# Kernel tuning notes

Measured on AMD Instinct MI355X. Metric: run time of the kernel, lower is better.

## Reference

```python
import jax, jax.numpy as jnp
import numpy as np

T = 20            # time_steps
BETA = 0.85
THR = 1.0         # snntorch Leaky default threshold
A_PRE = 0.005
A_POST = -0.003
STDP_INT = 3


@jax.custom_vjp
def spike_fn(mem_shift):
    # heaviside spike; backward uses snntorch atan surrogate (alpha=2)
    return (mem_shift > 0).astype(mem_shift.dtype)

def _spk_fwd(m):
    return (m > 0).astype(m.dtype), m

def _spk_bwd(m, g):
    # snntorch surrogate.atan, alpha=2: grad = g * (alpha/2) / (1 + (pi/2*alpha*U)^2) = g / (1 + (pi*U)^2)
    return (g / (1.0 + (jnp.pi * m) ** 2),)

spike_fn.defvjp(_spk_fwd, _spk_bwd)


def _lif(cur, mem):
    # snntorch Leaky (reset-by-subtraction): reset from previous mem (detached)
    reset = jax.lax.stop_gradient((mem > THR).astype(cur.dtype))
    mem = BETA * mem + cur - reset * THR
    spk = spike_fn(mem - THR)
    return spk, mem


def _snn_forward(x, embed, W1, b1, W2, b2, W3, b3, Wout, bout):
    B, S = x.shape
    H = W1.shape[0]
    x_emb = jnp.transpose(embed[x], (1, 0, 2))   # [S,B,E]
    x_rep = jnp.repeat(x_emb, T, axis=0)         # [S*T,B,E] (same embed for all 20 steps of a token)

    def step(carry, xe):
        mem1, mem2, mem3 = carry
        spk1, mem1 = _lif(xe @ W1.T + b1, mem1)
        spk2, mem2 = _lif(spk1 @ W2.T + b2, mem2)
        spk3, mem3 = _lif(spk2 @ W3.T + b3, mem3)
        return (mem1, mem2, mem3), (spk1, spk2, spk3)

    z = jnp.zeros((B, H), x_emb.dtype)
    (mem1, mem2, mem3), (spk1a, spk2a, spk3a) = jax.lax.scan(step, (z, z, z), x_rep)

    # STDP accumulation on steps where step % 3 == 0 (no-grad in original)
    mask = jnp.tile((jnp.arange(T) % STDP_INT == 0).astype(x_emb.dtype), S)  # [S*T]

    def stdp(pre, post):
        pre_m = jax.lax.stop_gradient(pre.mean(axis=1))    # [N, in]
        post_m = jax.lax.stop_gradient(post.mean(axis=1))  # [N, out]
        return jnp.einsum('n,no,ni->oi', mask, A_POST * post_m, A_PRE * pre_m)

    d1 = stdp(x_rep, spk1a)
    d2 = stdp(spk1a, spk2a)
    d3 = stdp(spk2a, spk3a)

    pooled = spk3a.reshape(S, T, B, H).mean(axis=1)  # mean over time_steps -> [S,B,H]
    out = jnp.transpose(pooled @ Wout.T + bout, (1, 0, 2))  # [B,S,V]
    rec1, rec2, rec3 = (jax.lax.stop_gradient(s) for s in (spk1a, spk2a, spk3a))
    return out, mem1, mem2, mem3, d1, d2, d3, rec1, rec2, rec3


def setup_inputs() -> dict:
    key = jax.random.key(0)
    ks = jax.random.split(key, 10)
    V, H, E, B, S = 32000, 256, 128, 32, 128
    inp = {
        'x': jax.random.randint(ks[0], (B, S), 0, V),
        'embed': jax.random.normal(ks[1], (V, E), jnp.float32),
        'W1': jax.random.normal(ks[2], (H, E), jnp.float32) * 0.08,
        'b1': jnp.zeros((H,), jnp.float32),
        'W2': jax.random.normal(ks[3], (H, H), jnp.float32) * 0.06,
        'b2': jnp.zeros((H,), jnp.float32),
        'W3': jax.random.normal(ks[4], (H, H), jnp.float32) * 0.06,
        'b3': jnp.zeros((H,), jnp.float32),
        'Wout': jax.random.normal(ks[5], (V, H), jnp.float32) * 0.06,
        'bout': jnp.zeros((V,), jnp.float32),
    }
    return inp


def reference(x, embed, W1, b1, W2, b2, W3, b3, Wout, bout):
    return _snn_forward(x, embed, W1, b1, W2, b2, W3, b3, Wout, bout)
```

## Files before the change

### kernel.cpp

```cpp
#include <hip/hip_runtime.h>
#include <cstdint>

#define T_STEPS 20
#define S_LEN   128
#define BATCH   32
#define HID     256
#define EMB     128
#define VOCAB   32000
#define NSTEP   (S_LEN*T_STEPS)
#define NBROWS  (NSTEP*BATCH)

typedef __bf16 bf8   __attribute__((ext_vector_type(8)));
typedef float  f32x4 __attribute__((ext_vector_type(4)));

static __device__ __forceinline__ unsigned short f2bf_u(float f){
  unsigned int u = __builtin_bit_cast(unsigned int, f);
  u = u + 0x7FFFu + ((u >> 16) & 1u);
  return (unsigned short)(u >> 16);
}

__global__ void k_f32_to_bf16(const float* __restrict__ src, unsigned short* __restrict__ dst, int n4){
  int i = blockIdx.x*blockDim.x + threadIdx.x;
  if (i < n4){
    float4 v = ((const float4*)src)[i];
    ushort4 o; o.x=f2bf_u(v.x); o.y=f2bf_u(v.y); o.z=f2bf_u(v.z); o.w=f2bf_u(v.w);
    ((ushort4*)dst)[i] = o;
  }
}

__global__ void k_wT(const float* __restrict__ W, float* __restrict__ WT){
  int i = blockIdx.x*blockDim.x + threadIdx.x;
  int n = i >> 8, k = i & 255;
  WT[k*HID + n] = W[i];
}

__global__ void k_xm(const int* __restrict__ x, const float* __restrict__ embed, float* __restrict__ Xm){
  int s = blockIdx.x, i = threadIdx.x;
  float acc = 0.f;
  for (int b=0;b<BATCH;b++){
    int tok = x[b*S_LEN + s];
    acc += embed[(size_t)tok*EMB + i];
  }
  Xm[s*EMB + i] = acc * (1.0f/32.0f);
}

__global__ __launch_bounds__(256) void k_cur1(const int* __restrict__ x, const float* __restrict__ embed,
                                              const float* __restrict__ W1, const float* __restrict__ b1,
                                              float* __restrict__ cur1){
  __shared__ float xe[BATCH*EMB];
  int s = blockIdx.x, t = threadIdx.x;
  for (int i=t; i<BATCH*EMB/4; i+=256){
    int b = i >> 5, e4 = i & 31;
    int tok = x[b*S_LEN + s];
    ((float4*)xe)[i] = ((const float4*)(embed + (size_t)tok*EMB))[e4];
  }
  __syncthreads();
  int h = t;
  float acc[BATCH];
  #pragma unroll
  for (int b=0;b<BATCH;b++) acc[b]=0.f;
  for (int ec=0; ec<4; ec++){
    float wd[32];
    #pragma unroll
    for (int e4=0;e4<8;e4++){
      float4 w = *(const float4*)(W1 + (size_t)h*EMB + ec*32 + e4*4);
      wd[e4*4+0]=w.x; wd[e4*4+1]=w.y; wd[e4*4+2]=w.z; wd[e4*4+3]=w.w;
    }
    #pragma unroll
    for (int b=0;b<BATCH;b++){
      #pragma unroll
      for (int e=0;e<32;e++)
        acc[b] = fmaf(xe[b*EMB + ec*32 + e], wd[e], acc[b]);
    }
  }
  float bi = b1[h];
  #pragma unroll
  for (int b=0;b<BATCH;b++)
    cur1[(size_t)(s*BATCH + b)*HID + h] = __fadd_rn(acc[b], bi);
}

__global__ __launch_bounds__(64) void k_scan1(const float* __restrict__ cur1, float* __restrict__ rec,
                                              float* __restrict__ memout){
  int bid = blockIdx.x; int b = bid >> 2; int hq = bid & 3;
  int h = hq*64 + threadIdx.x;
  const int strN = BATCH*HID;
  const float* cp = cur1 + b*HID + h;
  float* rp = rec + b*HID + h;
  float mem = 0.f;
  float c = cp[0];
  for (int s=0; s<S_LEN; s++){
    float cn = (s+1 < S_LEN) ? cp[(size_t)(s+1)*strN] : 0.f;
    #pragma unroll
    for (int t=0;t<T_STEPS;t++){
      float reset = (mem > 1.0f) ? 1.0f : 0.0f;
      float tm = __fmul_rn(0.85f, mem);
      tm = __fadd_rn(tm, c);
      mem = __fsub_rn(tm, reset);
      rp[(size_t)(s*T_STEPS + t)*strN] = (mem > 1.0f) ? 1.0f : 0.0f;
    }
    c = cn;
  }
  memout[b*HID + h] = mem;
}

template<bool POOL>
__global__ __launch_bounds__(64) void k_scan23(const float* __restrict__ cur,
                                               float* __restrict__ rec, float* __restrict__ memout,
                                               unsigned short* __restrict__ pooled){
  int bid = blockIdx.x; int b = bid >> 2; int hq = bid & 3;
  int h = hq*64 + threadIdx.x;
  const int strN = BATCH*HID;
  const float* cp = cur + b*HID + h;
  float* rp = rec + b*HID + h;
  unsigned short* pp = POOL ? (pooled + (size_t)b*S_LEN*HID + h) : nullptr;
  float mem = 0.f;
  float ps = 0.f;
  int tc = 0, sTok = 0;
  float cA[16], cB[16];

  auto step = [&](float c, int n){
    float reset = (mem > 1.0f) ? 1.0f : 0.0f;
    float tm = __fmul_rn(0.85f, mem);
    tm = __fadd_rn(tm, c);
    mem = __fsub_rn(tm, reset);
    float spk = (mem > 1.0f) ? 1.f : 0.f;
    rp[(size_t)n*strN] = spk;
    if constexpr (POOL){
      ps += spk;
      if (++tc == T_STEPS){
        pp[(size_t)sTok*HID] = f2bf_u(__fdiv_rn(ps, 20.0f));
        ps = 0.f; tc = 0; ++sTok;
      }
    }
  };

  #pragma unroll
  for (int j=0;j<16;j++) cA[j] = cp[(size_t)j*strN];
  for (int n0=0; n0<NSTEP; n0+=32){
    #pragma unroll
    for (int j=0;j<16;j++) cB[j] = cp[(size_t)(n0+16+j)*strN];
    #pragma unroll
    for (int j=0;j<16;j++) step(cA[j], n0+j);
    if (n0+32 < NSTEP){
      #pragma unroll
      for (int j=0;j<16;j++) cA[j] = cp[(size_t)(n0+32+j)*strN];
    }
    #pragma unroll
    for (int j=0;j<16;j++) step(cB[j], n0+16+j);
  }
  memout[b*HID + h] = mem;
}

__global__ __launch_bounds__(256) void k_gemm_f32(const float* __restrict__ spk,
                                                  const float* __restrict__ WT,
                                                  const float* __restrict__ bias,
                                                  float* __restrict__ curo){
  __shared__ float As[256*36];
  int m0 = blockIdx.y * 256;
  int n0 = blockIdx.x * 32;
  int t  = threadIdx.x;
  float acc[32];
  #pragma unroll
  for (int n=0;n<32;n++) acc[n]=0.f;

  for (int kc=0; kc<8; kc++){
    __syncthreads();
    #pragma unroll
    for (int i=0;i<8;i++){
      int id = t + i*256;
      int r = id >> 3, c4 = id & 7;
      float4 v = *(const float4*)(spk + (size_t)(m0 + r)*HID + kc*32 + c4*4);
      *(float4*)(As + r*36 + c4*4) = v;
    }
    __syncthreads();
    const float* wrow = WT + (size_t)(kc*32)*HID + n0;
    #pragma unroll
    for (int g=0; g<8; g++){
      float4 sv4 = *(const float4*)(As + t*36 + g*4);
      #pragma unroll
      for (int j=0;j<4;j++){
        float sv = (j==0)?sv4.x:(j==1)?sv4.y:(j==2)?sv4.z:sv4.w;
        const float* wt = wrow + (size_t)(g*4+j)*HID;
        #pragma unroll
        for (int n=0;n<32;n++)
          acc[n] = fmaf(sv, wt[n], acc[n]);
      }
    }
  }
  float* op = curo + (size_t)(m0 + t)*HID + n0;
  #pragma unroll
  for (int n=0;n<32;n++) op[n] = __fadd_rn(acc[n], bias[n0+n]);
}

template<bool BF16B>
__global__ __launch_bounds__(256,2) void k_gemm_out(const unsigned short* __restrict__ Abf,
                                                    const unsigned short* __restrict__ Bbf,
                                                    const float* __restrict__ Bf32,
                                                    const float* __restrict__ bout,
                                                    float* __restrict__ outp){
  __shared__ unsigned short As[128*72];
  __shared__ unsigned short Bs[128*72];
  int bid = blockIdx.x;
  int ntile = bid >> 5;
  int mtile = bid & 31;
  int m0 = mtile*128, n0 = ntile*128;
  int tid = threadIdx.x;
  int lane = tid & 63, wave = tid >> 6;
  int wm = wave >> 1, wn = wave & 1;
  int lm = lane & 15, quad = lane >> 4;
  f32x4 acc[4][4] = {};

  for (int kt=0; kt<4; kt++){
    int k0 = kt*64;
    uint4 avb[4];
    #pragma unroll
    for (int i=0;i<4;i++){
      int id = tid + i*256; int r = id>>3, c16 = id&7;
      avb[i] = *(const uint4*)(Abf + (size_t)(m0 + r)*HID + k0 + c16*8);
    }
    uint4 bvb[4]; float4 bvf[8];
    if (BF16B){
      #pragma unroll
      for (int i=0;i<4;i++){
        int id = tid + i*256; int r = id>>3, c16 = id&7;
        bvb[i] = *(const uint4*)(Bbf + (size_t)(n0 + r)*HID + k0 + c16*8);
      }
    } else {
      #pragma unroll
      for (int i=0;i<8;i++){
        int id = tid + i*256; int r = id>>4, c4 = id&15;
        bvf[i] = *(const float4*)(Bf32 + (size_t)(n0 + r)*HID + k0 + c4*4);
      }
    }
    __syncthreads();
    #pragma unroll
    for (int i=0;i<4;i++){
      int id = tid + i*256; int r = id>>3, c16 = id&7;
      *(uint4*)(As + r*72 + c16*8) = avb[i];
    }
    if (BF16B){
      #pragma unroll
      for (int i=0;i<4;i++){
        int id = tid + i*256; int r = id>>3, c16 = id&7;
        *(uint4*)(Bs + r*72 + c16*8) = bvb[i];
      }
    } else {
      #pragma unroll
      for (int i=0;i<8;i++){
        int id = tid + i*256; int r = id>>4, c4 = id&15;
        ushort4 o; o.x=f2bf_u(bvf[i].x); o.y=f2bf_u(bvf[i].y); o.z=f2bf_u(bvf[i].z); o.w=f2bf_u(bvf[i].w);
        *(ushort4*)(Bs + r*72 + c4*4) = o;
      }
    }
    __syncthreads();
    bf8 af[4][2], bfr[4][2];
    #pragma unroll
    for (int mt=0;mt<4;mt++)
      #pragma unroll
      for (int kk=0;kk<2;kk++)
        af[mt][kk] = *(const bf8*)(As + (wm*64 + mt*16 + lm)*72 + kk*32 + quad*8);
    #pragma unroll
    for (int nt=0;nt<4;nt++)
      #pragma unroll
      for (int kk=0;kk<2;kk++)
        bfr[nt][kk] = *(const bf8*)(Bs + (wn*64 + nt*16 + lm)*72 + kk*32 + quad*8);
    #pragma unroll
    for (int mt=0;mt<4;mt++)
      #pragma unroll
      for (int nt=0;nt<4;nt++){
        acc[mt][nt] = __builtin_amdgcn_mfma_f32_16x16x32_bf16(af[mt][0], bfr[nt][0], acc[mt][nt], 0,0,0);
        acc[mt][nt] = __builtin_amdgcn_mfma_f32_16x16x32_bf16(af[mt][1], bfr[nt][1], acc[mt][nt], 0,0,0);
      }
    __syncthreads();
  }
  #pragma unroll
  for (int nt=0;nt<4;nt++){
    int v = n0 + wn*64 + nt*16 + lm;
    float bo = bout[v];
    #pragma unroll
    for (int mt=0;mt<4;mt++)
      #pragma unroll
      for (int rr=0;rr<4;rr++){
        int r = m0 + wm*64 + mt*16 + quad*4 + rr;
        outp[(size_t)r*VOCAB + v] = acc[mt][nt][rr] + bo;
      }
  }
}

__global__ void k_mmean(const float* __restrict__ rec, float* __restrict__ M){
  int m = blockIdx.x, o = threadIdx.x;
  int s = m / 7, j = m - 7*s;
  int n = s*T_STEPS + j*3;
  const float* rp = rec + (size_t)n*BATCH*HID + o;
  float acc = 0.f;
  #pragma unroll
  for (int b=0;b<BATCH;b++) acc += rp[b*HID];
  M[m*HID + o] = acc * (1.0f/32.0f);
}

__global__ void k_d1(const float* __restrict__ M1, const float* __restrict__ Xm, float* __restrict__ d1){
  __shared__ float col[896];
  int o = blockIdx.x, i = threadIdx.x;
  for (int m=i; m<896; m+=128) col[m] = M1[m*HID + o];
  __syncthreads();
  float acc = 0.f;
  for (int s=0;s<S_LEN;s++){
    float xv = Xm[s*EMB + i];
    float cs = 0.f;
    #pragma unroll
    for (int j=0;j<7;j++) cs += col[s*7+j];
    acc += cs * xv;
  }
  d1[o*EMB + i] = -1.5e-5f * acc;
}

__global__ void k_d23(const float* __restrict__ Mpost, const float* __restrict__ Mpre, float* __restrict__ d){
  __shared__ float col[896];
  int o = blockIdx.x, i = threadIdx.x;
  for (int m=i; m<896; m+=256) col[m] = Mpost[m*HID + o];
  __syncthreads();
  float acc = 0.f;
  for (int m=0;m<896;m++) acc += col[m] * Mpre[m*HID + i];
  d[o*HID + i] = -1.5e-5f * acc;
}

extern "C" void kernel_launch(void* const* d_in, const int* in_sizes, int n_in,
                              void* d_out, int out_size, void* d_ws, size_t ws_size,
                              hipStream_t stream){
  const int*   x     = (const int*)d_in[0];
  const float* embed = (const float*)d_in[1];
  const float* W1    = (const float*)d_in[2];
  const float* b1    = (const float*)d_in[3];
  const float* W2    = (const float*)d_in[4];
  const float* b2    = (const float*)d_in[5];
  const float* W3    = (const float*)d_in[6];
  const float* b3    = (const float*)d_in[7];
  const float* Wout  = (const float*)d_in[8];
  const float* bout  = (const float*)d_in[9];
  float* out = (float*)d_out;

  float* mem1 = out + 131072000;
  float* mem2 = out + 131080192;
  float* mem3 = out + 131088384;
  float* d1   = out + 131096576;
  float* d2   = out + 131129344;
  float* d3   = out + 131194880;
  float* rec1 = out + 131260416;
  float* rec2 = out + 152231936;
  float* rec3 = out + 173203456;

  float* curbuf = out + 0;
  float* cur1   = out + 20971520;
  float* Xm     = out + 22020096;
  float* M1     = out + 22036480;
  float* M2     = out + 22265856;
  float* M3     = out + 22495232;
  float* WT2    = out + 22724608;
  float* WT3    = out + 22790144;

  unsigned short* pooled = (unsigned short*)d_ws;
  bool haveWoutBf = ws_size >= (size_t)(2097152 + 16384000);
  unsigned short* woutbf = (unsigned short*)((char*)d_ws + 2097152);

  if (haveWoutBf)
    k_f32_to_bf16<<<8000,256,0,stream>>>(Wout, woutbf, VOCAB*HID/4);
  k_wT<<<256,256,0,stream>>>(W2, WT2);
  k_wT<<<256,256,0,stream>>>(W3, WT3);
  k_xm<<<128,128,0,stream>>>(x, embed, Xm);
  k_cur1<<<128,256,0,stream>>>(x, embed, W1, b1, cur1);

  k_scan1<<<128,64,0,stream>>>(cur1, rec1, mem1);
  k_gemm_f32<<<dim3(8,320),256,0,stream>>>(rec1, WT2, b2, curbuf);
  k_scan23<false><<<128,64,0,stream>>>(curbuf, rec2, mem2, nullptr);
  k_gemm_f32<<<dim3(8,320),256,0,stream>>>(rec2, WT3, b3, curbuf);
  k_scan23<true><<<128,64,0,stream>>>(curbuf, rec3, mem3, pooled);

  k_mmean<<<896,256,0,stream>>>(rec1, M1);
  k_mmean<<<896,256,0,stream>>>(rec2, M2);
  k_mmean<<<896,256,0,stream>>>(rec3, M3);
  k_d1<<<256,128,0,stream>>>(M1, Xm, d1);
  k_d23<<<256,256,0,stream>>>(M2, M1, d2);
  k_d23<<<256,256,0,stream>>>(M3, M2, d3);

  if (haveWoutBf)
    k_gemm_out<true ><<<8000,256,0,stream>>>(pooled, woutbf, nullptr, bout, out);
  else
    k_gemm_out<false><<<8000,256,0,stream>>>(pooled, nullptr, Wout,  bout, out);
}
```

Measured before the change: 1.966 ms.

## Fuse prep kernels, remap GEMM blocks per XCD, use nontemporal output stores

```diff
diff --git a/kernel.cpp b/kernel.cpp
--- a/kernel.cpp
+++ b/kernel.cpp
@@ -19,29 +19,36 @@
   return (unsigned short)(u >> 16);
 }
 
-__global__ void k_f32_to_bf16(const float* __restrict__ src, unsigned short* __restrict__ dst, int n4){
-  int i = blockIdx.x*blockDim.x + threadIdx.x;
-  if (i < n4){
-    float4 v = ((const float4*)src)[i];
+__global__ __launch_bounds__(256) void k_prep(const float* __restrict__ Wout, unsigned short* __restrict__ woutbf,
+                                              const float* __restrict__ W2, float* __restrict__ WT2,
+                                              const float* __restrict__ W3, float* __restrict__ WT3,
+                                              const int* __restrict__ x, const float* __restrict__ embed,
+                                              float* __restrict__ Xm, int base){
+  int blk = blockIdx.x + base;
+  int t = threadIdx.x;
+  if (blk < 8000){
+    int i = blk*256 + t;
+    float4 v = ((const float4*)Wout)[i];
     ushort4 o; o.x=f2bf_u(v.x); o.y=f2bf_u(v.y); o.z=f2bf_u(v.z); o.w=f2bf_u(v.w);
-    ((ushort4*)dst)[i] = o;
-  }
-}
-
-__global__ void k_wT(const float* __restrict__ W, float* __restrict__ WT){
-  int i = blockIdx.x*blockDim.x + threadIdx.x;
-  int n = i >> 8, k = i & 255;
-  WT[k*HID + n] = W[i];
-}
-
-__global__ void k_xm(const int* __restrict__ x, const float* __restrict__ embed, float* __restrict__ Xm){
-  int s = blockIdx.x, i = threadIdx.x;
-  float acc = 0.f;
-  for (int b=0;b<BATCH;b++){
-    int tok = x[b*S_LEN + s];
-    acc += embed[(size_t)tok*EMB + i];
-  }
-  Xm[s*EMB + i] = acc * (1.0f/32.0f);
+    ((ushort4*)woutbf)[i] = o;
+  } else if (blk < 8256){
+    int i = (blk-8000)*256 + t;
+    int n = i >> 8, k = i & 255;
+    WT2[k*HID + n] = W2[i];
+  } else if (blk < 8512){
+    int i = (blk-8256)*256 + t;
+    int n = i >> 8, k = i & 255;
+    WT3[k*HID + n] = W3[i];
+  } else {
+    int s = (blk-8512)*2 + (t >> 7);
+    int i = t & 127;
+    float acc = 0.f;
+    for (int b=0;b<BATCH;b++){
+      int tok = x[b*S_LEN + s];
+      acc += embed[(size_t)tok*EMB + i];
+    }
+    Xm[s*EMB + i] = acc * (1.0f/32.0f);
+  }
 }
 
 __global__ __launch_bounds__(256) void k_cur1(const int* __restrict__ x, const float* __restrict__ embed,
@@ -156,8 +163,11 @@
                                                   const float* __restrict__ bias,
                                                   float* __restrict__ curo){
   __shared__ float As[256*36];
-  int m0 = blockIdx.y * 256;
-  int n0 = blockIdx.x * 32;
+  int bid = blockIdx.x;
+  int x = bid & 7, i = bid >> 3;
+  int w = x*320 + i;
+  int m0 = (w >> 3) * 256;
+  int n0 = (w & 7) * 32;
   int t  = threadIdx.x;
   float acc[32];
   #pragma unroll
@@ -166,8 +176,8 @@
   for (int kc=0; kc<8; kc++){
     __syncthreads();
     #pragma unroll
-    for (int i=0;i<8;i++){
-      int id = t + i*256;
+    for (int j=0;j<8;j++){
+      int id = t + j*256;
       int r = id >> 3, c4 = id & 7;
       float4 v = *(const float4*)(spk + (size_t)(m0 + r)*HID + kc*32 + c4*4);
       *(float4*)(As + r*36 + c4*4) = v;
@@ -201,8 +211,10 @@
   __shared__ unsigned short As[128*72];
   __shared__ unsigned short Bs[128*72];
   int bid = blockIdx.x;
-  int ntile = bid >> 5;
-  int mtile = bid & 31;
+  int xc = bid & 7, ib = bid >> 3;
+  int w = xc*1000 + ib;
+  int ntile = w >> 5;
+  int mtile = w & 31;
   int m0 = mtile*128, n0 = ntile*128;
   int tid = threadIdx.x;
   int lane = tid & 63, wave = tid >> 6;
@@ -282,7 +294,7 @@
       #pragma unroll
       for (int rr=0;rr<4;rr++){
         int r = m0 + wm*64 + mt*16 + quad*4 + rr;
-        outp[(size_t)r*VOCAB + v] = acc[mt][nt][rr] + bo;
+        __builtin_nontemporal_store(acc[mt][nt][rr] + bo, &outp[(size_t)r*VOCAB + v]);
       }
   }
 }
@@ -362,17 +374,14 @@
   bool haveWoutBf = ws_size >= (size_t)(2097152 + 16384000);
   unsigned short* woutbf = (unsigned short*)((char*)d_ws + 2097152);
 
-  if (haveWoutBf)
-    k_f32_to_bf16<<<8000,256,0,stream>>>(Wout, woutbf, VOCAB*HID/4);
-  k_wT<<<256,256,0,stream>>>(W2, WT2);
-  k_wT<<<256,256,0,stream>>>(W3, WT3);
-  k_xm<<<128,128,0,stream>>>(x, embed, Xm);
+  int base = haveWoutBf ? 0 : 8000;
+  k_prep<<<8576-base,256,0,stream>>>(Wout, woutbf, W2, WT2, W3, WT3, x, embed, Xm, base);
   k_cur1<<<128,256,0,stream>>>(x, embed, W1, b1, cur1);
 
   k_scan1<<<128,64,0,stream>>>(cur1, rec1, mem1);
-  k_gemm_f32<<<dim3(8,320),256,0,stream>>>(rec1, WT2, b2, curbuf);
+  k_gemm_f32<<<2560,256,0,stream>>>(rec1, WT2, b2, curbuf);
   k_scan23<false><<<128,64,0,stream>>>(curbuf, rec2, mem2, nullptr);
-  k_gemm_f32<<<dim3(8,320),256,0,stream>>>(rec2, WT3, b3, curbuf);
+  k_gemm_f32<<<2560,256,0,stream>>>(rec2, WT3, b3, curbuf);
   k_scan23<true><<<128,64,0,stream>>>(curbuf, rec3, mem3, pooled);
 
   k_mmean<<<896,256,0,stream>>>(rec1, M1);
```

New measurement: 1.922 ms. 1.02x faster.
